# Optimization experiments

Measured on AMD Instinct MI355X. Metric: run time of the kernel, lower is better.

Reference implementation:

```python
import jax, jax.numpy as jnp
import numpy as np
import math

N_PATHS = 2048
N_STEPS = 512
N_FWD = 40
N_FACTORS = 3
H = 0.1
ALPHA = H - 0.5            # fBM kernel exponent
BETA_SABR = 0.5
SHIFT = 0.02
DT = 1.0 / N_STEPS
GAMMA_CONST = math.gamma(H + 0.5)
BETA_DECAY = 0.05


def setup_inputs() -> dict:
    key = jax.random.key(0)
    tenors = np.linspace(0.0, 10.0, N_FWD + 1)
    T = tenors[:-1]
    tau = np.diff(tenors).astype(np.float32)
    F0 = np.full(N_FWD, 0.02, dtype=np.float32)
    # alphas = base normal vols / |F0+shift|^beta  (as in __init__)
    base_vols = np.full(N_FWD, 0.006)
    eta_F0 = np.abs(F0 + SHIFT) ** BETA_SABR
    alphas = (base_vols / eta_F0).astype(np.float32)
    rhos = np.full(N_FWD, -0.3, dtype=np.float32)
    nus = np.full(N_FWD, 0.5, dtype=np.float32)
    # PCA loadings from exponential spatial correlation (as in __init__)
    corr = np.exp(-BETA_DECAY * np.abs(T[:, None] - T[None, :]))
    evals, evecs = np.linalg.eigh(corr)
    idx = np.argsort(evals)[::-1][:N_FACTORS]
    L = evecs[:, idx] * np.sqrt(np.clip(evals[idx], 0.0, None))[None, :]
    L = L / np.sqrt((L ** 2).sum(axis=1, keepdims=True))
    Lam = np.triu(L @ L.T, 1).astype(np.float32)
    # Brownian increments, pre-scaled by sqrt(dt) (replaces Sobol+icdf draw)
    dz = jax.random.normal(key, (N_PATHS, N_STEPS, N_FACTORS + 1), dtype=jnp.float32) * float(np.sqrt(DT))
    return {
        "dz_all": dz,
        "F0": jnp.asarray(F0),
        "alphas": jnp.asarray(alphas),
        "rhos": jnp.asarray(rhos),
        "nus": jnp.asarray(nus),
        "tau": jnp.asarray(tau),
        "loadings": jnp.asarray(L.astype(np.float32)),
        "Lambda_upper": jnp.asarray(Lam),
    }


def reference(dz_all, F0, alphas, rhos, nus, tau, loadings, Lambda_upper):
    n_paths, n_steps, _ = dz_all.shape
    dtype = dz_all.dtype
    # --- hybrid-scheme Volterra / fBM kernel [n_steps, n_steps] ---
    idx = jnp.arange(n_steps)
    k = jnp.maximum(idx[:, None] - idx[None, :] + 1, 0).astype(dtype)
    # with b_eval='optimal', riemann == exact weights, so the where(k<=kappa) is identity
    exact_w = (k ** (ALPHA + 1.0) - jnp.maximum(k - 1.0, 0.0) ** (ALPHA + 1.0)) / (ALPHA + 1.0)
    kernel = jnp.where(idx[:, None] >= idx[None, :], exact_w * (DT ** ALPHA) / GAMMA_CONST, 0.0)
    # variance compensator [N, n_steps]
    var_comp = 0.5 * (nus ** 2)[:, None] * jnp.sum(kernel ** 2, axis=1)[None, :] * DT
    # --- correlated Brownian drivers and fBM via kernel convolution ---
    wr = jnp.einsum('psf,nf->psn', dz_all[..., :N_FACTORS], loadings)          # [P,S,N]
    fbm4 = jnp.einsum('ts,psd->ptd', kernel, dz_all)                            # [P,S,4]
    fbm_curve = jnp.einsum('ptf,nf->ptn', fbm4[..., :N_FACTORS], loadings)      # [P,S,N]
    fbm = rhos * fbm_curve + jnp.sqrt(1.0 - rhos ** 2) * fbm4[..., -1:]
    unit_vols = jnp.exp(nus * fbm - var_comp.T[None])                            # [P,S,N]
    v2_dt = unit_vols ** 2 * DT
    # --- frozen-drift forward dynamics ---
    eta_f0 = jnp.abs(F0 + SHIFT) ** BETA_SABR
    vol_scale = alphas * eta_f0
    omega_0 = tau * vol_scale / (1.0 + tau * F0)
    mu_0 = -vol_scale * (Lambda_upper @ omega_0)
    dF = mu_0 * v2_dt + wr * (unit_vols * vol_scale)
    F_path = F0 + jnp.cumsum(dF, axis=1)                                         # [P,S,N]
    return jnp.concatenate([jnp.broadcast_to(F0, (n_paths, 1, F0.shape[0])), F_path], axis=1)
```

## Files before the change

### kernel.cpp

```cpp
#include <hip/hip_runtime.h>
#include <math.h>

#define NS 512
#define NF 40
#define ROWS_OUT 513
#define DTC (1.0f / 512.0f)
#define PLANE 520


__global__ __launch_bounds__(64) void const_kernel(
    const float* __restrict__ F0, const float* __restrict__ alphas,
    const float* __restrict__ rhos, const float* __restrict__ nus,
    const float* __restrict__ tau, const float* __restrict__ L,
    const float* __restrict__ Lam, float* __restrict__ ws)
{
    __shared__ double wd[NS];
    __shared__ float omega0[NF];
    __shared__ float vs_s[NF];
    int n = threadIdx.x;

    {
        const double g06 = 1.4891922488128171;
        const double dta = pow(512.0, 0.4);
        #pragma unroll
        for (int k = 0; k < 8; ++k) {
            int m = n * 8 + k;
            double wv = (pow((double)m + 1.0, 0.6) - pow((double)m, 0.6)) * (1.0 / 0.6) * dta / g06;
            wd[m] = wv;
            ws[m] = (float)wv;
        }
    }
    if (n < NF) {
        float f0 = F0[n];
        float vs = alphas[n] * sqrtf(fabsf(f0 + 0.02f));
        vs_s[n] = vs;
        omega0[n] = tau[n] * vs / (1.0f + tau[n] * f0);
    }
    __syncthreads();
    if (n == 0) {
        double acc = 0.0;
        for (int m = 0; m < NS; ++m) { acc += wd[m] * wd[m]; ws[NS + m] = (float)acc; }
    }
    if (n < NF) {
        float s = 0.0f;
        for (int j = 0; j < NF; ++j) s += Lam[n * NF + j] * omega0[j];
        float vs = vs_s[n];
        float mu0 = -vs * s;
        float rho = rhos[n], nu = nus[n];
        float* c = ws + 1024 + n * 8;
        c[0] = vs * L[n * 3 + 0];
        c[1] = vs * L[n * 3 + 1];
        c[2] = vs * L[n * 3 + 2];
        c[3] = nu * rho / fmaxf(vs, 1e-30f);
        c[4] = nu * sqrtf(fmaxf(1.0f - rho * rho, 0.0f));
        c[5] = 0.5f * nu * nu * DTC;
        c[6] = mu0 * DTC;
        c[7] = F0[n];
    }
}

template<int CTRL, int RM>
__device__ __forceinline__ float dpp_add(float v) {
    int t = __builtin_amdgcn_update_dpp(0, __float_as_int(v), CTRL, RM, 0xf, true);
    return v + __int_as_float(t);
}
__device__ __forceinline__ float wave_iscan(float v) {
    v = dpp_add<0x111, 0xf>(v);
    v = dpp_add<0x112, 0xf>(v);
    v = dpp_add<0x114, 0xf>(v);
    v = dpp_add<0x118, 0xf>(v);
    v = dpp_add<0x142, 0xa>(v);
    v = dpp_add<0x143, 0xc>(v);
    return v;
}

__device__ __forceinline__ void fma4(float4& acc, float c, const float4& v) {
    acc.x = fmaf(c, v.x, acc.x);
    acc.y = fmaf(c, v.y, acc.y);
    acc.z = fmaf(c, v.z, acc.z);
    acc.w = fmaf(c, v.w, acc.w);
}

__global__ __launch_bounds__(256, 4) void path_kernel(
    const float* __restrict__ dz, const float* __restrict__ ws,
    float* __restrict__ out)
{
    __shared__ float planes[2 * 4 * PLANE];
    __shared__ float wp[768];
    __shared__ float cw2[NS];
    __shared__ float chunk[64 * 41];

    int tid = threadIdx.x;
    int lane = tid & 63;
    int wv = __builtin_amdgcn_readfirstlane(tid >> 6);
    int pA = blockIdx.x * 2, pB = pA + 1;
    const float4* dzgA = (const float4*)dz + (size_t)pA * NS;
    const float4* dzgB = (const float4*)dz + (size_t)pB * NS;

    for (int i = tid; i < 768; i += 256) wp[i] = (i < 256) ? 0.0f : ws[i - 256];
    for (int i = tid; i < NS; i += 256) cw2[i] = ws[NS + i];
    __syncthreads();

    {
        int role = (wv + (blockIdx.x & 3)) & 3;
        int path = role >> 1;
        int half = role & 1;
        int i = half * 64 + lane;
        int gmax = half ? 128 : 64;
        const float4* dzg = path ? dzgB : dzgA;
        float* pf = planes + path * 4 * PLANE;
        const float4* wp4 = (const float4*)wp;
        float4 a0 = make_float4(0.f, 0.f, 0.f, 0.f);
        float4 a1 = a0, a2 = a0, a3 = a0;
        float4 hi = wp4[64 + i];
        #pragma unroll 2
        for (int g = 0; g < gmax; ++g) {
            float4 d0 = dzg[4 * g + 0];
            float4 d1 = dzg[4 * g + 1];
            float4 d2 = dzg[4 * g + 2];
            float4 d3 = dzg[4 * g + 3];
            float4 lo = wp4[63 + i - g];
            fma4(a0, hi.x, d0); fma4(a1, hi.y, d0); fma4(a2, hi.z, d0); fma4(a3, hi.w, d0);
            fma4(a0, lo.w, d1); fma4(a1, hi.x, d1); fma4(a2, hi.y, d1); fma4(a3, hi.z, d1);
            fma4(a0, lo.z, d2); fma4(a1, lo.w, d2); fma4(a2, hi.x, d2); fma4(a3, hi.y, d2);
            fma4(a0, lo.y, d3); fma4(a1, lo.z, d3); fma4(a2, lo.w, d3); fma4(a3, hi.x, d3);
            hi = lo;
        }
        ((float4*)(pf + 0 * PLANE))[i] = make_float4(a0.x, a1.x, a2.x, a3.x);
        ((float4*)(pf + 1 * PLANE))[i] = make_float4(a0.y, a1.y, a2.y, a3.y);
        ((float4*)(pf + 2 * PLANE))[i] = make_float4(a0.z, a1.z, a2.z, a3.z);
        ((float4*)(pf + 3 * PLANE))[i] = make_float4(a0.w, a1.w, a2.w, a3.w);
    }

    float carryA[10], carryB[10];
    #pragma unroll
    for (int j = 0; j < 10; ++j) { carryA[j] = 0.0f; carryB[j] = 0.0f; }

    float* outA = out + (size_t)pA * (ROWS_OUT * NF);
    float* outB = out + (size_t)pB * (ROWS_OUT * NF);
    if (tid < NF) outA[tid] = ws[1024 + tid * 8 + 7];
    if (tid >= 64 && tid < 64 + NF) outB[tid - 64] = ws[1024 + (tid - 64) * 8 + 7];

    __syncthreads();

    for (int cix = 0; cix < 8; ++cix) {
        int t = cix * 64 + lane;
        float cw = cw2[t];
        #pragma unroll
        for (int path = 0; path < 2; ++path) {
            const float* pf = planes + path * 4 * PLANE;
            float fx = pf[t], fy = pf[PLANE + t], fz = pf[2 * PLANE + t], fw = pf[3 * PLANE + t];
            float4 d = path ? dzgB[t] : dzgA[t];
            float* carry = path ? carryB : carryA;
            #pragma unroll
            for (int j = 0; j < 10; ++j) {
                int n = wv * 10 + j;
                const float* c = ws + 1024 + n * 8;
                float cC0 = c[0], cC1 = c[1], cC2 = c[2], q = c[3];
                float cA3 = c[4], ca = c[5], cm0 = c[6], f0 = c[7];
                float dotf = fx * cC0 + fy * cC1 + fz * cC2;
                float arg = fmaf(q, dotf, fmaf(cA3, fw, -ca * cw));
                float uv = __expf(arg);
                float dotc = d.x * cC0 + d.y * cC1 + d.z * cC2;
                float dF = uv * fmaf(cm0, uv, dotc);
                float v = wave_iscan(dF) + carry[j];
                carry[j] = __int_as_float(__builtin_amdgcn_readlane(__float_as_int(v), 63));
                chunk[lane * 41 + n] = v + f0;
            }
            __syncthreads();
            float* o = (path ? outB : outA) + NF + cix * (64 * NF);
            #pragma unroll
            for (int k = 0; k < 10; ++k) {
                int f = tid + k * 256;
                __builtin_nontemporal_store(chunk[f + f / 40], o + f);
            }
            __syncthreads();
        }
    }
}

extern "C" void kernel_launch(void* const* d_in, const int* in_sizes, int n_in,
                              void* d_out, int out_size, void* d_ws, size_t ws_size,
                              hipStream_t stream) {
    const float* dz   = (const float*)d_in[0];
    const float* F0   = (const float*)d_in[1];
    const float* alph = (const float*)d_in[2];
    const float* rhos = (const float*)d_in[3];
    const float* nus  = (const float*)d_in[4];
    const float* tau  = (const float*)d_in[5];
    const float* L    = (const float*)d_in[6];
    const float* Lam  = (const float*)d_in[7];
    float* ws = (float*)d_ws;
    float* out = (float*)d_out;

    int n_paths = in_sizes[0] / (NS * 4);

    const_kernel<<<1, 64, 0, stream>>>(F0, alph, rhos, nus, tau, L, Lam, ws);
    path_kernel<<<n_paths / 2, 256, 0, stream>>>(dz, ws, out);
}
```

Baseline: 283.5 us.

## Assign one path per block and split convolution work across four waves

Each block now handles a single path instead of two, so there are twice as many blocks, and launch bounds target eight blocks per CU. The fBM convolution for that one path is split among the four waves by segment of the reduction range, and the two partial sums are combined through shared memory. Shared memory shrinks because the weight table and the output staging buffer now share one region, and cw2 is read from global memory. The change aims at better load balance and more occupancy, at the cost of two extra barriers and reloading the weight table twice as often overall.

```diff
diff --git a/kernel.cpp b/kernel.cpp
--- a/kernel.cpp
+++ b/kernel.cpp
@@ -5,7 +5,7 @@
 #define NF 40
 #define ROWS_OUT 513
 #define DTC (1.0f / 512.0f)
-#define PLANE 520
+#define PLANE 512
 
 
 __global__ __launch_bounds__(64) void const_kernel(
@@ -81,101 +81,106 @@
     acc.w = fmaf(c, v.w, acc.w);
 }
 
-__global__ __launch_bounds__(256, 4) void path_kernel(
+__global__ __launch_bounds__(256, 8) void path_kernel(
     const float* __restrict__ dz, const float* __restrict__ ws,
     float* __restrict__ out)
 {
-    __shared__ float planes[2 * 4 * PLANE];
-    __shared__ float wp[768];
-    __shared__ float cw2[NS];
-    __shared__ float chunk[64 * 41];
+    __shared__ float planes[4 * PLANE];
+    __shared__ float ustage[64 * 41];
 
     int tid = threadIdx.x;
     int lane = tid & 63;
     int wv = __builtin_amdgcn_readfirstlane(tid >> 6);
-    int pA = blockIdx.x * 2, pB = pA + 1;
-    const float4* dzgA = (const float4*)dz + (size_t)pA * NS;
-    const float4* dzgB = (const float4*)dz + (size_t)pB * NS;
-
+    int p = blockIdx.x;
+    const float4* dzg = (const float4*)dz + (size_t)p * NS;
+
+    float* wp = ustage;
     for (int i = tid; i < 768; i += 256) wp[i] = (i < 256) ? 0.0f : ws[i - 256];
-    for (int i = tid; i < NS; i += 256) cw2[i] = ws[NS + i];
     __syncthreads();
 
     {
-        int role = (wv + (blockIdx.x & 3)) & 3;
-        int path = role >> 1;
-        int half = role & 1;
+        int role = (wv + p) & 3;
+        int half = role >> 1;
+        int seg  = role & 1;
         int i = half * 64 + lane;
-        int gmax = half ? 128 : 64;
-        const float4* dzg = path ? dzgB : dzgA;
-        float* pf = planes + path * 4 * PLANE;
+        int span = half ? 64 : 32;
+        int g0 = seg * span, g1 = g0 + span;
         const float4* wp4 = (const float4*)wp;
         float4 a0 = make_float4(0.f, 0.f, 0.f, 0.f);
         float4 a1 = a0, a2 = a0, a3 = a0;
-        float4 hi = wp4[64 + i];
         #pragma unroll 2
-        for (int g = 0; g < gmax; ++g) {
+        for (int g = g0; g < g1; ++g) {
             float4 d0 = dzg[4 * g + 0];
             float4 d1 = dzg[4 * g + 1];
             float4 d2 = dzg[4 * g + 2];
             float4 d3 = dzg[4 * g + 3];
             float4 lo = wp4[63 + i - g];
+            float4 hi = wp4[64 + i - g];
             fma4(a0, hi.x, d0); fma4(a1, hi.y, d0); fma4(a2, hi.z, d0); fma4(a3, hi.w, d0);
             fma4(a0, lo.w, d1); fma4(a1, hi.x, d1); fma4(a2, hi.y, d1); fma4(a3, hi.z, d1);
             fma4(a0, lo.z, d2); fma4(a1, lo.w, d2); fma4(a2, hi.x, d2); fma4(a3, hi.y, d2);
             fma4(a0, lo.y, d3); fma4(a1, lo.z, d3); fma4(a2, lo.w, d3); fma4(a3, hi.x, d3);
-            hi = lo;
-        }
-        ((float4*)(pf + 0 * PLANE))[i] = make_float4(a0.x, a1.x, a2.x, a3.x);
-        ((float4*)(pf + 1 * PLANE))[i] = make_float4(a0.y, a1.y, a2.y, a3.y);
-        ((float4*)(pf + 2 * PLANE))[i] = make_float4(a0.z, a1.z, a2.z, a3.z);
-        ((float4*)(pf + 3 * PLANE))[i] = make_float4(a0.w, a1.w, a2.w, a3.w);
-    }
-
-    float carryA[10], carryB[10];
+        }
+        if (seg == 1) {
+            ((float4*)(planes + 0 * PLANE))[i] = make_float4(a0.x, a1.x, a2.x, a3.x);
+            ((float4*)(planes + 1 * PLANE))[i] = make_float4(a0.y, a1.y, a2.y, a3.y);
+            ((float4*)(planes + 2 * PLANE))[i] = make_float4(a0.z, a1.z, a2.z, a3.z);
+            ((float4*)(planes + 3 * PLANE))[i] = make_float4(a0.w, a1.w, a2.w, a3.w);
+        }
+        __syncthreads();
+        if (seg == 0) {
+            float4* q0 = &((float4*)(planes + 0 * PLANE))[i];
+            float4* q1 = &((float4*)(planes + 1 * PLANE))[i];
+            float4* q2 = &((float4*)(planes + 2 * PLANE))[i];
+            float4* q3 = &((float4*)(planes + 3 * PLANE))[i];
+            float4 c0 = *q0, c1 = *q1, c2 = *q2, c3 = *q3;
+            c0.x += a0.x; c0.y += a1.x; c0.z += a2.x; c0.w += a3.x;
+            c1.x += a0.y; c1.y += a1.y; c1.z += a2.y; c1.w += a3.y;
+            c2.x += a0.z; c2.y += a1.z; c2.z += a2.z; c2.w += a3.z;
+            c3.x += a0.w; c3.y += a1.w; c3.z += a2.w; c3.w += a3.w;
+            *q0 = c0; *q1 = c1; *q2 = c2; *q3 = c3;
+        }
+        __syncthreads();
+    }
+
+    float carry[10];
     #pragma unroll
-    for (int j = 0; j < 10; ++j) { carryA[j] = 0.0f; carryB[j] = 0.0f; }
-
-    float* outA = out + (size_t)pA * (ROWS_OUT * NF);
-    float* outB = out + (size_t)pB * (ROWS_OUT * NF);
-    if (tid < NF) outA[tid] = ws[1024 + tid * 8 + 7];
-    if (tid >= 64 && tid < 64 + NF) outB[tid - 64] = ws[1024 + (tid - 64) * 8 + 7];
-
-    __syncthreads();
-
+    for (int j = 0; j < 10; ++j) carry[j] = 0.0f;
+
+    float* outP = out + (size_t)p * (ROWS_OUT * NF);
+    if (tid < NF) outP[tid] = ws[1024 + tid * 8 + 7];
+
+    float* chunk = ustage;
+    const float* cwg = ws + NS;
     for (int cix = 0; cix < 8; ++cix) {
         int t = cix * 64 + lane;
-        float cw = cw2[t];
+        float cw = cwg[t];
+        float fx = planes[t], fy = planes[PLANE + t];
+        float fz = planes[2 * PLANE + t], fw = planes[3 * PLANE + t];
+        float4 d = dzg[t];
         #pragma unroll
-        for (int path = 0; path < 2; ++path) {
-            const float* pf = planes + path * 4 * PLANE;
-            float fx = pf[t], fy = pf[PLANE + t], fz = pf[2 * PLANE + t], fw = pf[3 * PLANE + t];
-            float4 d = path ? dzgB[t] : dzgA[t];
-            float* carry = path ? carryB : carryA;
-            #pragma unroll
-            for (int j = 0; j < 10; ++j) {
-                int n = wv * 10 + j;
-                const float* c = ws + 1024 + n * 8;
-                float cC0 = c[0], cC1 = c[1], cC2 = c[2], q = c[3];
-                float cA3 = c[4], ca = c[5], cm0 = c[6], f0 = c[7];
-                float dotf = fx * cC0 + fy * cC1 + fz * cC2;
-                float arg = fmaf(q, dotf, fmaf(cA3, fw, -ca * cw));
-                float uv = __expf(arg);
-                float dotc = d.x * cC0 + d.y * cC1 + d.z * cC2;
-                float dF = uv * fmaf(cm0, uv, dotc);
-                float v = wave_iscan(dF) + carry[j];
-                carry[j] = __int_as_float(__builtin_amdgcn_readlane(__float_as_int(v), 63));
-                chunk[lane * 41 + n] = v + f0;
-            }
-            __syncthreads();
-            float* o = (path ? outB : outA) + NF + cix * (64 * NF);
-            #pragma unroll
-            for (int k = 0; k < 10; ++k) {
-                int f = tid + k * 256;
-                __builtin_nontemporal_store(chunk[f + f / 40], o + f);
-            }
-            __syncthreads();
-        }
+        for (int j = 0; j < 10; ++j) {
+            int n = wv * 10 + j;
+            const float* c = ws + 1024 + n * 8;
+            float cC0 = c[0], cC1 = c[1], cC2 = c[2], q = c[3];
+            float cA3 = c[4], ca = c[5], cm0 = c[6], f0 = c[7];
+            float dotf = fx * cC0 + fy * cC1 + fz * cC2;
+            float arg = fmaf(q, dotf, fmaf(cA3, fw, -ca * cw));
+            float uv = __expf(arg);
+            float dotc = d.x * cC0 + d.y * cC1 + d.z * cC2;
+            float dF = uv * fmaf(cm0, uv, dotc);
+            float v = wave_iscan(dF) + carry[j];
+            carry[j] = __int_as_float(__builtin_amdgcn_readlane(__float_as_int(v), 63));
+            chunk[lane * 41 + n] = v + f0;
+        }
+        __syncthreads();
+        float* o = outP + NF + cix * (64 * NF);
+        #pragma unroll
+        for (int k = 0; k < 10; ++k) {
+            int f = tid + k * 256;
+            __builtin_nontemporal_store(chunk[f + f / 40], o + f);
+        }
+        __syncthreads();
     }
 }
 
@@ -196,5 +201,5 @@
     int n_paths = in_sizes[0] / (NS * 4);
 
     const_kernel<<<1, 64, 0, stream>>>(F0, alph, rhos, nus, tau, L, Lam, ws);
-    path_kernel<<<n_paths / 2, 256, 0, stream>>>(dz, ws, out);
-}
+    path_kernel<<<n_paths, 256, 0, stream>>>(dz, ws, out);
+}
```

Result: faster. 256.2 us (-9.6%).
